# Optimization experiments

Hardware: AMD Instinct MI355X
Metric: run time of the kernel (lower is better)

The kernel has to match this reference:

```python
import jax, jax.numpy as jnp
import numpy as np

FEAT_STRIDE = 16
PRE_NMS = 6000   # TEST config
POST_NMS = 300
NMS_TH = 0.7


def _generate_anchors_3d(base_size=16, ratios=(0.5, 1.0, 2.0), scales=(8, 16, 32), time_dims=(16,)):
    """Standard Faster-RCNN anchor enumeration, extended with a time extent.
    Returns (A, 6) float32 boxes in [x1, y1, z1, x2, y2, z2] order (matches shift order)."""
    w = h = float(base_size)
    xc = yc = 0.5 * (base_size - 1)
    size = w * h
    ratios = np.asarray(ratios, dtype=np.float64)
    ws = np.round(np.sqrt(size / ratios))
    hs = np.round(ws * ratios)
    a2 = []
    for wi, hi in zip(ws, hs):
        for s in scales:
            ww, hh = wi * s, hi * s
            a2.append([xc - 0.5 * (ww - 1), yc - 0.5 * (hh - 1),
                       xc + 0.5 * (ww - 1), yc + 0.5 * (hh - 1)])
    out = []
    for t in time_dims:
        for a in a2:
            out.append([a[0], a[1], 0.0, a[2], a[3], float(t) - 1.0])
    return np.asarray(out, dtype=np.float32)


def setup_inputs() -> dict:
    key = jax.random.key(0)
    k1, k2 = jax.random.split(key)
    B, A, H, W, T = 2, 9, 32, 32, 16
    scores_map = jax.random.normal(k1, (B, 2 * A, H, W, T), dtype=jnp.float32)
    bbox_frame = jax.random.normal(k2, (B, 6 * A, H, W, T), dtype=jnp.float32) * 0.2
    im_info = jnp.array([512.0, 512.0, 16.0], dtype=jnp.float32)  # [img_h, img_w, n_frames]
    anchors = jnp.asarray(_generate_anchors_3d())  # (9, 6)
    return {"scores_map": scores_map, "bbox_frame": bbox_frame, "im_info": im_info, "anchors": anchors}


def _nms_single(boxes, scs):
    """Greedy 3D (spatio-temporal volume) NMS for one image.
    boxes: (N, 6), scs: (N,). Returns (POST_NMS, 7) rows [score, x1,y1,z1,x2,y2,z2],
    zero-padded past the number of kept proposals (matches output[i].zero_() + fill)."""
    order = jnp.argsort(-scs)[:PRE_NMS]           # descending score, pre-NMS top-k
    b = boxes[order]                              # (P, 6)
    s = scs[order]                                # (P,)
    vol = (b[:, 3] - b[:, 0] + 1.0) * (b[:, 4] - b[:, 1] + 1.0) * (b[:, 5] - b[:, 2] + 1.0)
    iw = jnp.clip(jnp.minimum(b[:, None, 3], b[None, :, 3]) - jnp.maximum(b[:, None, 0], b[None, :, 0]) + 1.0, 0.0)
    ih = jnp.clip(jnp.minimum(b[:, None, 4], b[None, :, 4]) - jnp.maximum(b[:, None, 1], b[None, :, 1]) + 1.0, 0.0)
    il = jnp.clip(jnp.minimum(b[:, None, 5], b[None, :, 5]) - jnp.maximum(b[:, None, 2], b[None, :, 2]) + 1.0, 0.0)
    inter = iw * ih * il                          # (P, P)
    iou = inter / (vol[:, None] + vol[None, :] - inter)
    iou = jax.lax.stop_gradient(iou)              # keep mask is non-differentiable
    P = b.shape[0]
    idx = jnp.arange(P)

    def step(keep, i):
        sup = (iou[i] > NMS_TH) & keep[i] & (idx > i)
        return keep & ~sup, None

    keep, _ = jax.lax.scan(step, jnp.ones((P,), dtype=bool), jnp.arange(P))
    rank = jnp.cumsum(keep) - 1
    pos = jnp.where(keep & (rank < POST_NMS), rank, POST_NMS)  # overflow slot POST_NMS
    rows = jnp.concatenate([s[:, None], b], axis=1)            # (P, 7)
    out = jnp.zeros((POST_NMS + 1, 7), dtype=boxes.dtype).at[pos].set(rows)
    return out[:POST_NMS]


def reference(scores_map, bbox_frame, im_info, anchors):
    A = anchors.shape[0]
    B = scores_map.shape[0]
    scores = scores_map[:, A:]                    # (B, A, H, W, T) foreground scores
    H, W, T = scores.shape[2], scores.shape[3], scores.shape[4]

    # --- anchor grid (matches np.meshgrid 'xy' + ravel = H-major, W, T order) ---
    sx = (jnp.arange(W) * FEAT_STRIDE).astype(scores_map.dtype)
    sy = (jnp.arange(H) * FEAT_STRIDE).astype(scores_map.dtype)
    sz = jnp.arange(T).astype(scores_map.dtype)
    X, Y, Z = jnp.meshgrid(sx, sy, sz)            # each (H, W, T)
    shift = jnp.stack([X.ravel(), Y.ravel(), Z.ravel()], axis=1)   # (K, 3)
    shifts = jnp.concatenate([shift, shift], axis=1)               # (K, 6)
    all_anchors = (anchors[None] + shifts[:, None]).reshape(-1, 6)  # (K*A, 6)

    deltas = bbox_frame.transpose(0, 2, 3, 4, 1).reshape(B, -1, 6)  # (B, K*A, 6)
    scs = scores.transpose(0, 2, 3, 4, 1).reshape(B, -1)            # (B, K*A)

    # --- bbox_transform_inv_3d ---
    aw = all_anchors[:, 3] - all_anchors[:, 0] + 1.0
    ah = all_anchors[:, 4] - all_anchors[:, 1] + 1.0
    al = all_anchors[:, 5] - all_anchors[:, 2] + 1.0
    acx = all_anchors[:, 0] + 0.5 * aw
    acy = all_anchors[:, 1] + 0.5 * ah
    acz = all_anchors[:, 2] + 0.5 * al
    pcx = deltas[..., 0] * aw + acx
    pcy = deltas[..., 1] * ah + acy
    pcz = deltas[..., 2] * al + acz
    pw = jnp.exp(deltas[..., 3]) * aw
    ph = jnp.exp(deltas[..., 4]) * ah
    pl = jnp.exp(deltas[..., 5]) * al
    proposals = jnp.stack([pcx - 0.5 * pw, pcy - 0.5 * ph, pcz - 0.5 * pl,
                           pcx + 0.5 * pw, pcy + 0.5 * ph, pcz + 0.5 * pl], axis=-1)

    # --- clip_boxes_3d: x in [0, img_w-1], y in [0, img_h-1], z in [0, n_frames-1] ---
    lim = jnp.stack([im_info[1], im_info[0], im_info[2],
                     im_info[1], im_info[0], im_info[2]]) - 1.0
    proposals = jnp.clip(proposals, 0.0, lim)

    return jax.vmap(_nms_single)(proposals, scs)  # (B, POST_NMS, 7)
```

## Files before the change

kernel.cpp:

```cpp
#include <hip/hip_runtime.h>
#include <stdint.h>

#define FEAT_STRIDE 16
#define PRE_NMS 6000
#define POST_NMS 300
#define NMS_TH 0.7f

static constexpr int B_ = 2, A_ = 9, H_ = 32, W_ = 32, T_ = 16;
static constexpr int LOC = H_ * W_ * T_;
static constexpr int N_ = LOC * A_;
static constexpr int NBIN = 65536;
static constexpr int NREP = 8;
static constexpr int CAP = 8192;
static constexpr int NW = 94;
static constexpr int ROWS = 6016;

static constexpr double BMID = 0.7000000178813934326171875;


__device__ __forceinline__ uint32_t f2u(float f) {
    uint32_t b = __float_as_uint(f);
    return b ^ ((b >> 31) ? 0xFFFFFFFFu : 0x80000000u);
}
__device__ __forceinline__ float u2f(uint32_t u) {
    uint32_t b = (u >> 31) ? (u ^ 0x80000000u) : ~u;
    return __uint_as_float(b);
}

__global__ void hist_kernel(const float* __restrict__ scores_map,
                            unsigned int* __restrict__ histR) {
    int gid = blockIdx.x * blockDim.x + threadIdx.x;
    if (gid >= B_ * N_) return;
    int b = gid / N_;
    int r = gid - b * N_;
    int a = r / LOC;
    int loc = r - a * LOC;
    float sc = scores_map[((size_t)(b * 2 * A_ + A_ + a)) * LOC + loc];
    uint32_t u = f2u(sc);
    int rep = blockIdx.x & (NREP - 1);
    atomicAdd(&histR[((size_t)(rep * B_ + b)) * NBIN + (u >> 16)], 1u);
}

__global__ void __launch_bounds__(256) partial_kernel(
        const unsigned int* __restrict__ histR,
        unsigned int* __restrict__ partials) {
    int c = blockIdx.x, bb = blockIdx.y, t = threadIdx.x;
    unsigned int s = 0;
#pragma unroll
    for (int r = 0; r < NREP; ++r) {
        const uint4* h4 = reinterpret_cast<const uint4*>(
            histR + ((size_t)(r * B_ + bb)) * NBIN + c * 1024);
        uint4 v = h4[t];
        s += v.x + v.y + v.z + v.w;
    }
    __shared__ unsigned int red[256];
    red[t] = s;
    __syncthreads();
    for (int off = 128; off > 0; off >>= 1) {
        if (t < off) red[t] += red[t + off];
        __syncthreads();
    }
    if (t == 0) partials[bb * 64 + c] = red[0];
}

__global__ void __launch_bounds__(256) rewrite_kernel(
        const unsigned int* __restrict__ histR,
        unsigned int* __restrict__ hist,
        unsigned int* __restrict__ binbase,
        const unsigned int* __restrict__ partials,
        unsigned int* __restrict__ thr) {
    int c = blockIdx.x, bb = blockIdx.y, t = threadIdx.x;
    __shared__ unsigned int sp[64];
    __shared__ unsigned int ssum[256];
    if (t < 64) sp[t] = partials[bb * 64 + t];
    uint4 v = {0u, 0u, 0u, 0u};
#pragma unroll
    for (int r = 0; r < NREP; ++r) {
        const uint4* h4 = reinterpret_cast<const uint4*>(
            histR + ((size_t)(r * B_ + bb)) * NBIN + c * 1024);
        uint4 w = h4[t];
        v.x += w.x; v.y += w.y; v.z += w.z; v.w += w.w;
    }
    unsigned int* h = hist + (size_t)bb * NBIN + c * 1024;
    unsigned int* bs = binbase + (size_t)bb * NBIN + c * 1024;
    ssum[t] = v.x + v.y + v.z + v.w;
    __syncthreads();
    unsigned int chunkBase = 0;
    for (int q = c + 1; q < 64; ++q) chunkBase += sp[q];
    for (int off = 1; off < 256; off <<= 1) {
        unsigned int val = (t + off < 256) ? ssum[t + off] : 0u;
        __syncthreads();
        ssum[t] += val;
        __syncthreads();
    }
    unsigned int run = chunkBase + ((t < 255) ? ssum[t + 1] : 0u);
    unsigned int cnt[4] = {v.x, v.y, v.z, v.w};
    unsigned int offv[4];
    for (int q = 3; q >= 0; --q) {
        offv[q] = run;
        unsigned int newrun = run + cnt[q];
        if (run < (unsigned)PRE_NMS && newrun >= (unsigned)PRE_NMS) {
            thr[bb * 2 + 0] = (unsigned)(c * 1024 + t * 4 + q);
            thr[bb * 2 + 1] = newrun;
        }
        run = newrun;
    }
    uint4 o4 = {offv[0], offv[1], offv[2], offv[3]};
    reinterpret_cast<uint4*>(h)[t] = o4;
    reinterpret_cast<uint4*>(bs)[t] = o4;
}

__global__ void __launch_bounds__(256) compact_kernel(
        const float* __restrict__ scores_map,
        const unsigned int* __restrict__ thr,
        unsigned long long* __restrict__ cand,
        unsigned int* __restrict__ hist) {
    int tid = threadIdx.x;
    int gid = blockIdx.x * 256 + tid;
    int b = gid / N_;
    int r = gid - b * N_;
    int a = r / LOC;
    int loc = r - a * LOC;
    float sc = scores_map[((size_t)(b * 2 * A_ + A_ + a)) * LOC + loc];
    uint32_t u = f2u(sc);
    uint32_t bin = u >> 16;
    if (bin >= thr[b * 2]) {
        int n = loc * A_ + a;
        unsigned long long key = ((unsigned long long)u << 18)
                               | (unsigned long long)(N_ - 1 - n);
        unsigned int slot = atomicAdd(&hist[b * NBIN + bin], 1u);
        if (slot < (unsigned)CAP)
            cand[(size_t)b * CAP + slot] = key;
    }
}

__global__ void __launch_bounds__(256) bucket_decode(
        const unsigned long long* __restrict__ cand,
        const unsigned int* __restrict__ hist,
        const unsigned int* __restrict__ binbase,
        const unsigned int* __restrict__ thr,
        const float* __restrict__ bbox_frame,
        const float* __restrict__ im_info,
        const float* __restrict__ anchors,
        float* __restrict__ sortedBox) {
    int gid = blockIdx.x * 256 + threadIdx.x;
    int bb = gid / CAP;
    int i = gid - bb * CAP;
    int count = (int)thr[bb * 2 + 1];
    if (count > CAP) count = CAP;
    if (i >= count) return;
    const unsigned long long* cb = cand + (size_t)bb * CAP;
    unsigned long long me = cb[i];
    int bin = (int)(me >> 34);
    int start = (int)binbase[bb * NBIN + bin];
    int end = (int)hist[bb * NBIN + bin];
    if (end > count) end = count;
    int rank = start;
    for (int q = start; q < end; ++q)
        rank += (cb[q] > me);
    if (rank >= PRE_NMS) return;

    uint32_t u = (uint32_t)(me >> 18);
    int n = N_ - 1 - (int)(me & 0x3FFFFull);
    int a = n % A_;
    int loc = n / A_;
    int k = loc % T_;
    int j = (loc / T_) % W_;
    int ii = loc / (T_ * W_);

    float ax1 = anchors[a * 6 + 0] + (float)(FEAT_STRIDE * j);
    float ay1 = anchors[a * 6 + 1] + (float)(FEAT_STRIDE * ii);
    float az1 = anchors[a * 6 + 2] + (float)k;
    float ax2 = anchors[a * 6 + 3] + (float)(FEAT_STRIDE * j);
    float ay2 = anchors[a * 6 + 4] + (float)(FEAT_STRIDE * ii);
    float az2 = anchors[a * 6 + 5] + (float)k;
    float aw = ax2 - ax1 + 1.0f, ah = ay2 - ay1 + 1.0f, al = az2 - az1 + 1.0f;
    float acx = ax1 + 0.5f * aw, acy = ay1 + 0.5f * ah, acz = az1 + 0.5f * al;

    const float* dp = bbox_frame + ((size_t)(bb * 6 * A_ + a * 6)) * LOC
                    + ii * (W_ * T_) + j * T_ + k;
    float d0 = dp[0 * LOC], d1 = dp[1 * LOC], d2 = dp[2 * LOC];
    float d3 = dp[3 * LOC], d4 = dp[4 * LOC], d5 = dp[5 * LOC];

    float pcx = d0 * aw + acx, pcy = d1 * ah + acy, pcz = d2 * al + acz;
    float pw = expf(d3) * aw, ph = expf(d4) * ah, pl = expf(d5) * al;

    float x1 = pcx - 0.5f * pw, y1 = pcy - 0.5f * ph, z1 = pcz - 0.5f * pl;
    float x2 = pcx + 0.5f * pw, y2 = pcy + 0.5f * ph, z2 = pcz + 0.5f * pl;

    float lx = im_info[1] - 1.0f, ly = im_info[0] - 1.0f, lz = im_info[2] - 1.0f;
    x1 = fminf(fmaxf(x1, 0.0f), lx); y1 = fminf(fmaxf(y1, 0.0f), ly); z1 = fminf(fmaxf(z1, 0.0f), lz);
    x2 = fminf(fmaxf(x2, 0.0f), lx); y2 = fminf(fmaxf(y2, 0.0f), ly); z2 = fminf(fmaxf(z2, 0.0f), lz);

    float vol = (x2 - x1 + 1.0f) * (y2 - y1 + 1.0f) * (z2 - z1 + 1.0f);
    float* p = sortedBox + ((size_t)bb * ROWS + rank) * 8;
    p[0] = x1; p[1] = y1; p[2] = z1; p[3] = x2;
    p[4] = y2; p[5] = z2; p[6] = vol; p[7] = u2f(u);
}

__global__ void mask_build(const float* __restrict__ sortedBox,
                           unsigned long long* __restrict__ mask,
                           unsigned long long* __restrict__ diagBand) {
    int g = blockIdx.x / NW, w = blockIdx.x % NW;
    if (w < g) return;
    int bb = blockIdx.y;
    int lane = threadIdx.x;
    __shared__ float4 colA[64];
    __shared__ float4 colB[64];
    const float* sb = sortedBox + (size_t)bb * ROWS * 8;
    int col = w * 64 + lane;
    if (col < PRE_NMS) {
        const float4* cp4 = reinterpret_cast<const float4*>(sb + (size_t)col * 8);
        float4 lo = cp4[0], hi = cp4[1];
        colA[lane] = make_float4(lo.x, lo.y, lo.z, lo.w);
        colB[lane] = make_float4(hi.x, hi.y, hi.z, 0.0f);
    } else {
        colA[lane] = make_float4(3e8f, 0.0f, 0.0f, -3e8f);
        colB[lane] = make_float4(0.0f, 0.0f, 1.0f, 0.0f);
    }
    __syncthreads();
    int row = g * 64 + lane;
    if (row >= PRE_NMS) return;
    const float4* rp4 = reinterpret_cast<const float4*>(sb + (size_t)row * 8);
    float4 rlo = rp4[0], rhi = rp4[1];
    float x1 = rlo.x, y1 = rlo.y, z1 = rlo.z;
    float x2 = rlo.w, y2 = rhi.x, z2 = rhi.y, v = rhi.z;
    unsigned long long word = 0;
#pragma unroll 8
    for (int b2 = 0; b2 < 64; ++b2) {
        float4 cA = colA[b2];
        float4 cB = colB[b2];
        float iw = fminf(x2, cA.w) - fmaxf(x1, cA.x) + 1.0f;
        float ih = fminf(y2, cB.x) - fmaxf(y1, cA.y) + 1.0f;
        float il = fminf(z2, cB.y) - fmaxf(z1, cA.z) + 1.0f;
        iw = fmaxf(iw, 0.0f); ih = fmaxf(ih, 0.0f); il = fmaxf(il, 0.0f);
        float inter = iw * ih * il;
        float denom = v + cB.z - inter;
        bool over = ((double)inter >= BMID * (double)denom);
        int cidx = w * 64 + b2;
        if (cidx > row && over) word |= (1ull << b2);
    }
    mask[((size_t)bb * NW + w) * ROWS + row] = word;
    if (w == g) {
        diagBand[((size_t)bb * ROWS + row) * 2 + 0] = word;
        if (g == NW - 1) diagBand[((size_t)bb * ROWS + row) * 2 + 1] = 0ull;
    }
    if (w == g + 1) diagBand[((size_t)bb * ROWS + row) * 2 + 1] = word;
}

__global__ void __launch_bounds__(1024) suppress_kernel(
        const unsigned long long* __restrict__ mask,
        const unsigned long long* __restrict__ diagBand,
        const float* __restrict__ sortedBox,
        float* __restrict__ out) {
    int bb = blockIdx.x;
    int tid = threadIdx.x;
    int lane = tid & 63;
    __shared__ unsigned long long remv[NW];
    __shared__ int kr[2][64];
    __shared__ int s_nk;
    for (int i = tid; i < NW; i += 1024) remv[i] = 0ull;
    if (tid == 0) {
        remv[NW - 1] = ~((1ull << (PRE_NMS - (NW - 1) * 64)) - 1ull);
        s_nk = 0;
    }
    __syncthreads();

    const unsigned long long* M = mask + (size_t)bb * NW * ROWS;
    const unsigned long long* D = diagBand + (size_t)bb * ROWS * 2;
    const float* sb = sortedBox + (size_t)bb * ROWS * 8;
    float* ob = out + (size_t)bb * POST_NMS * 7;

    int kept_total = 0, prev_nk = 0, prev_base = 0, cur = 0;
    unsigned long long diag0 = 0, band1 = 0, sup = 0;
    if (tid < 64) {
        diag0 = D[lane * 2 + 0];
        band1 = D[lane * 2 + 1];
    }

    for (int c = 0; c < NW; ++c) {
        unsigned long long nxt0 = 0, nxt1 = 0;
        if (tid < 64) {
            if (c + 1 < NW) {
                nxt0 = D[((c + 1) * 64 + lane) * 2 + 0];
                nxt1 = D[((c + 1) * 64 + lane) * 2 + 1];
            }
            unsigned long long alive = ~(remv[c] | sup);
            unsigned long long supn = 0;
            int nk = 0;
            while (alive && kept_total + nk < POST_NMS) {
                int b = __builtin_ctzll(alive);
                if (lane == 0) kr[cur][nk] = c * 64 + b;
                ++nk;
                alive &= ~(__shfl(diag0, b) | (1ull << b));
                supn |= __shfl(band1, b);
            }
            sup = supn;
            if (tid == 0) s_nk = nk;
        } else {
            int t = tid - 64;
            for (int w2 = c + 1 + t; w2 < NW; w2 += 960) {
                unsigned long long vv = remv[w2];
                for (int i = 0; i < prev_nk; ++i)
                    vv |= M[(size_t)w2 * ROWS + kr[cur ^ 1][i]];
                remv[w2] = vv;
            }
            for (int e = t; e < prev_nk * 7; e += 960) {
                int i = e / 7, j = e - i * 7;
                ob[(size_t)(prev_base + i) * 7 + j] =
                    sb[(size_t)kr[cur ^ 1][i] * 8 + (j == 0 ? 7 : j - 1)];
            }
        }
        __syncthreads();
        int nk = s_nk;
        prev_base = kept_total;
        kept_total += nk;
        prev_nk = nk;
        cur ^= 1;
        if (tid < 64) { diag0 = nxt0; band1 = nxt1; }
        if (kept_total >= POST_NMS) break;
    }
    for (int e = tid; e < prev_nk * 7; e += 1024) {
        int i = e / 7, j = e - i * 7;
        ob[(size_t)(prev_base + i) * 7 + j] =
            sb[(size_t)kr[cur ^ 1][i] * 8 + (j == 0 ? 7 : j - 1)];
    }
    for (int idx = kept_total * 7 + tid; idx < POST_NMS * 7; idx += 1024)
        ob[idx] = 0.0f;
}

extern "C" void kernel_launch(void* const* d_in, const int* in_sizes, int n_in,
                              void* d_out, int out_size, void* d_ws, size_t ws_size,
                              hipStream_t stream) {
    const float* scores_map = (const float*)d_in[0];
    const float* bbox_frame = (const float*)d_in[1];
    const float* im_info    = (const float*)d_in[2];
    const float* anchors    = (const float*)d_in[3];
    float* out = (float*)d_out;

    char* ws = (char*)d_ws;
    unsigned long long* mask     = (unsigned long long*)(ws + 0);
    unsigned int* binbase        = (unsigned int*)(ws + 0);
    unsigned int* histR          = (unsigned int*)(ws + 524288);
    float* sortedBox             = (float*)(ws + 9048064);
    unsigned long long* cand     = (unsigned long long*)(ws + 9433088);
    unsigned int* hist           = (unsigned int*)(ws + 9564160);
    unsigned long long* diagBand = (unsigned long long*)(ws + 9564160);
    unsigned int* thr            = (unsigned int*)(ws + 10088448);
    unsigned int* partials       = (unsigned int*)(ws + 10088464);

    hipMemsetAsync(histR, 0, (size_t)NREP * B_ * NBIN * 4, stream);

    int total = B_ * N_;
    hist_kernel<<<(total + 255) / 256, 256, 0, stream>>>(scores_map, histR);
    partial_kernel<<<dim3(64, B_), 256, 0, stream>>>(histR, partials);
    rewrite_kernel<<<dim3(64, B_), 256, 0, stream>>>(histR, hist, binbase, partials, thr);
    compact_kernel<<<total / 256, 256, 0, stream>>>(scores_map, thr, cand, hist);
    bucket_decode<<<B_ * CAP / 256, 256, 0, stream>>>(cand, hist, binbase, thr,
                                                      bbox_frame, im_info, anchors,
                                                      sortedBox);
    mask_build<<<dim3(NW * NW, B_), 64, 0, stream>>>(sortedBox, mask, diagBand);
    suppress_kernel<<<B_, 1024, 0, stream>>>(mask, diagBand, sortedBox, out);
}
```

Measured before the change: 134.1 us.

## Pipeline NMS suppress loop with a two-word band and deferred mask merging

The diagonal band grows to three 64-bit words per row, so suppression from the next two chunks is handled inside the 64-lane wave. That frees the other threads to fetch mask words for a chunk one iteration early and OR them into shared remv one iteration later with LDS atomics. The serial greedy loop now uses readfirstlane/readlane instead of shuffles and a raw s_barrier. Output rows are written once at the end from a shared kept-index list. This removes global-load latency and output writes from the critical serial path, at the cost of a larger band buffer and more register state.

Measured after the change: 138.6 us. +3.3%, slower.

```diff
diff --git a/kernel.cpp b/kernel.cpp
--- a/kernel.cpp
+++ b/kernel.cpp
@@ -25,6 +25,11 @@
 __device__ __forceinline__ float u2f(uint32_t u) {
     uint32_t b = (u >> 31) ? (u ^ 0x80000000u) : ~u;
     return __uint_as_float(b);
+}
+__device__ __forceinline__ unsigned long long rl64(unsigned long long v, int lane) {
+    unsigned int lo = (unsigned int)__builtin_amdgcn_readlane((int)(unsigned int)v, lane);
+    unsigned int hi = (unsigned int)__builtin_amdgcn_readlane((int)(unsigned int)(v >> 32), lane);
+    return ((unsigned long long)hi << 32) | lo;
 }
 
 __global__ void hist_kernel(const float* __restrict__ scores_map,
@@ -200,7 +205,7 @@
 
 __global__ void mask_build(const float* __restrict__ sortedBox,
                            unsigned long long* __restrict__ mask,
-                           unsigned long long* __restrict__ diagBand) {
+                           unsigned long long* __restrict__ band) {
     int g = blockIdx.x / NW, w = blockIdx.x % NW;
     if (w < g) return;
     int bb = blockIdx.y;
@@ -241,91 +246,122 @@
         if (cidx > row && over) word |= (1ull << b2);
     }
     mask[((size_t)bb * NW + w) * ROWS + row] = word;
+    unsigned long long* bd = band + ((size_t)bb * ROWS + row) * 4;
     if (w == g) {
-        diagBand[((size_t)bb * ROWS + row) * 2 + 0] = word;
-        if (g == NW - 1) diagBand[((size_t)bb * ROWS + row) * 2 + 1] = 0ull;
-    }
-    if (w == g + 1) diagBand[((size_t)bb * ROWS + row) * 2 + 1] = word;
+        bd[0] = word;
+        if (g + 1 >= NW) bd[1] = 0ull;
+        if (g + 2 >= NW) bd[2] = 0ull;
+    }
+    if (w == g + 1) bd[1] = word;
+    if (w == g + 2) bd[2] = word;
 }
 
 __global__ void __launch_bounds__(1024) suppress_kernel(
         const unsigned long long* __restrict__ mask,
-        const unsigned long long* __restrict__ diagBand,
+        const unsigned long long* __restrict__ band,
         const float* __restrict__ sortedBox,
         float* __restrict__ out) {
     int bb = blockIdx.x;
     int tid = threadIdx.x;
     int lane = tid & 63;
     __shared__ unsigned long long remv[NW];
-    __shared__ int kr[2][64];
-    __shared__ int s_nk;
+    __shared__ int kr[3][64];
+    __shared__ int keptAll[POST_NMS];
+    __shared__ int snk[3];
+    __shared__ int stot[2];
     for (int i = tid; i < NW; i += 1024) remv[i] = 0ull;
     if (tid == 0) {
         remv[NW - 1] = ~((1ull << (PRE_NMS - (NW - 1) * 64)) - 1ull);
-        s_nk = 0;
+        snk[0] = snk[1] = snk[2] = 0;
     }
     __syncthreads();
 
-    const unsigned long long* M = mask + (size_t)bb * NW * ROWS;
-    const unsigned long long* D = diagBand + (size_t)bb * ROWS * 2;
+    const unsigned long long* M  = mask + (size_t)bb * NW * ROWS;
+    const unsigned long long* Bd = band + (size_t)bb * ROWS * 4;
     const float* sb = sortedBox + (size_t)bb * ROWS * 8;
     float* ob = out + (size_t)bb * POST_NMS * 7;
 
-    int kept_total = 0, prev_nk = 0, prev_base = 0, cur = 0;
-    unsigned long long diag0 = 0, band1 = 0, sup = 0;
+    unsigned long long d0 = 0, d1 = 0, d2 = 0;
+    unsigned long long supCur = 0, S1 = 0, S2 = 0;
+    unsigned long long pend[8];
+    int kept_total = 0;
     if (tid < 64) {
-        diag0 = D[lane * 2 + 0];
-        band1 = D[lane * 2 + 1];
-    }
-
+        const ulonglong2* bp = reinterpret_cast<const ulonglong2*>(&Bd[(size_t)lane * 4]);
+        ulonglong2 v01 = bp[0], v23 = bp[1];
+        d0 = v01.x; d1 = v01.y; d2 = v23.x;
+    }
+
+    int total = 0;
     for (int c = 0; c < NW; ++c) {
-        unsigned long long nxt0 = 0, nxt1 = 0;
         if (tid < 64) {
+            unsigned long long n0 = 0, n1 = 0, n2 = 0;
             if (c + 1 < NW) {
-                nxt0 = D[((c + 1) * 64 + lane) * 2 + 0];
-                nxt1 = D[((c + 1) * 64 + lane) * 2 + 1];
+                const ulonglong2* bp = reinterpret_cast<const ulonglong2*>(
+                    &Bd[(size_t)((c + 1) * 64 + lane) * 4]);
+                ulonglong2 v01 = bp[0], v23 = bp[1];
+                n0 = v01.x; n1 = v01.y; n2 = v23.x;
             }
-            unsigned long long alive = ~(remv[c] | sup);
-            unsigned long long supn = 0;
+            unsigned long long alive = ~(remv[c] | supCur);
             int nk = 0;
             while (alive && kept_total + nk < POST_NMS) {
-                int b = __builtin_ctzll(alive);
-                if (lane == 0) kr[cur][nk] = c * 64 + b;
+                int b = (int)__builtin_ctzll(alive);
+                int bs = __builtin_amdgcn_readfirstlane(b);
+                unsigned long long dr = rl64(d0, bs);
+                if (lane == 0) {
+                    kr[c % 3][nk] = c * 64 + bs;
+                    keptAll[kept_total + nk] = c * 64 + bs;
+                }
+                S1 |= rl64(d1, bs);
+                S2 |= rl64(d2, bs);
                 ++nk;
-                alive &= ~(__shfl(diag0, b) | (1ull << b));
-                supn |= __shfl(band1, b);
+                alive &= ~(dr | (1ull << bs));
             }
-            sup = supn;
-            if (tid == 0) s_nk = nk;
+            kept_total += nk;
+            if (lane == 0) { snk[c % 3] = nk; stot[c & 1] = kept_total; }
+            supCur = S1; S1 = S2; S2 = 0;
+            d0 = n0; d1 = n1; d2 = n2;
         } else {
             int t = tid - 64;
-            for (int w2 = c + 1 + t; w2 < NW; w2 += 960) {
-                unsigned long long vv = remv[w2];
-                for (int i = 0; i < prev_nk; ++i)
-                    vv |= M[(size_t)w2 * ROWS + kr[cur ^ 1][i]];
-                remv[w2] = vv;
+            int wi = t >> 3, s = t & 7;
+            if (c >= 2) {
+                int t2 = c - 2;
+                int w = t2 + 3 + wi;
+                int nk2 = snk[t2 % 3];
+                if (w < NW && s < nk2) {
+                    unsigned long long acc = 0;
+#pragma unroll
+                    for (int q = 0; q < 8; ++q) {
+                        int i = s + q * 8;
+                        if (i < nk2) acc |= pend[q];
+                    }
+                    atomicOr(&remv[w], acc);
+                }
             }
-            for (int e = t; e < prev_nk * 7; e += 960) {
-                int i = e / 7, j = e - i * 7;
-                ob[(size_t)(prev_base + i) * 7 + j] =
-                    sb[(size_t)kr[cur ^ 1][i] * 8 + (j == 0 ? 7 : j - 1)];
+            if (c >= 1) {
+                int t1 = c - 1;
+                int w = t1 + 3 + wi;
+                int nk1 = snk[t1 % 3];
+                if (w < NW) {
+#pragma unroll
+                    for (int q = 0; q < 8; ++q) {
+                        int i = s + q * 8;
+                        if (i < nk1) pend[q] = M[(size_t)w * ROWS + kr[t1 % 3][i]];
+                    }
+                }
             }
         }
-        __syncthreads();
-        int nk = s_nk;
-        prev_base = kept_total;
-        kept_total += nk;
-        prev_nk = nk;
-        cur ^= 1;
-        if (tid < 64) { diag0 = nxt0; band1 = nxt1; }
-        if (kept_total >= POST_NMS) break;
-    }
-    for (int e = tid; e < prev_nk * 7; e += 1024) {
+        asm volatile("s_waitcnt lgkmcnt(0)" ::: "memory");
+        __builtin_amdgcn_s_barrier();
+        asm volatile("" ::: "memory");
+        total = stot[c & 1];
+        if (total >= POST_NMS) break;
+    }
+
+    for (int e = tid; e < total * 7; e += 1024) {
         int i = e / 7, j = e - i * 7;
-        ob[(size_t)(prev_base + i) * 7 + j] =
-            sb[(size_t)kr[cur ^ 1][i] * 8 + (j == 0 ? 7 : j - 1)];
-    }
-    for (int idx = kept_total * 7 + tid; idx < POST_NMS * 7; idx += 1024)
+        ob[e] = sb[(size_t)keptAll[i] * 8 + (j == 0 ? 7 : j - 1)];
+    }
+    for (int idx = total * 7 + tid; idx < POST_NMS * 7; idx += 1024)
         ob[idx] = 0.0f;
 }
 
@@ -339,15 +375,15 @@
     float* out = (float*)d_out;
 
     char* ws = (char*)d_ws;
-    unsigned long long* mask     = (unsigned long long*)(ws + 0);
-    unsigned int* binbase        = (unsigned int*)(ws + 0);
-    unsigned int* histR          = (unsigned int*)(ws + 524288);
-    float* sortedBox             = (float*)(ws + 9048064);
-    unsigned long long* cand     = (unsigned long long*)(ws + 9433088);
-    unsigned int* hist           = (unsigned int*)(ws + 9564160);
-    unsigned long long* diagBand = (unsigned long long*)(ws + 9564160);
-    unsigned int* thr            = (unsigned int*)(ws + 10088448);
-    unsigned int* partials       = (unsigned int*)(ws + 10088464);
+    unsigned long long* mask  = (unsigned long long*)(ws + 0);
+    unsigned int* binbase     = (unsigned int*)(ws + 0);
+    unsigned int* histR       = (unsigned int*)(ws + 524288);
+    float* sortedBox          = (float*)(ws + 9048064);
+    unsigned long long* cand  = (unsigned long long*)(ws + 9433088);
+    unsigned int* hist        = (unsigned int*)(ws + 9564160);
+    unsigned long long* band  = (unsigned long long*)(ws + 9564160);
+    unsigned int* thr         = (unsigned int*)(ws + 10088448);
+    unsigned int* partials    = (unsigned int*)(ws + 10088464);
 
     hipMemsetAsync(histR, 0, (size_t)NREP * B_ * NBIN * 4, stream);
 
@@ -359,6 +395,6 @@
     bucket_decode<<<B_ * CAP / 256, 256, 0, stream>>>(cand, hist, binbase, thr,
                                                       bbox_frame, im_info, anchors,
                                                       sortedBox);
-    mask_build<<<dim3(NW * NW, B_), 64, 0, stream>>>(sortedBox, mask, diagBand);
-    suppress_kernel<<<B_, 1024, 0, stream>>>(mask, diagBand, sortedBox, out);
-}
+    mask_build<<<dim3(NW * NW, B_), 64, 0, stream>>>(sortedBox, mask, band);
+    suppress_kernel<<<B_, 1024, 0, stream>>>(mask, band, sortedBox, out);
+}
```

## Process two mask words per suppress iteration and fuse histogram replica merge

Applied to the files above, without the earlier changes.

The greedy NMS suppress loop now handles two 64-column words per block-wide iteration, which halves the number of __syncthreads barriers on the serial critical path. To make that work, mask_build writes a 4-word band per row, so suppression from the previous pair reaches both current words. The greedy wave uses readfirstlane/readlane instead of shuffles. Separately, partial_kernel now writes the merged histogram so rewrite_kernel no longer re-reads all 8 replicas. The cost is more register state, a larger band buffer, and a longer serial inner step per iteration.

Result: slower. 136.9 us (+2.1%).

```diff
diff --git a/kernel.cpp b/kernel.cpp
--- a/kernel.cpp
+++ b/kernel.cpp
@@ -25,6 +25,11 @@
 __device__ __forceinline__ float u2f(uint32_t u) {
     uint32_t b = (u >> 31) ? (u ^ 0x80000000u) : ~u;
     return __uint_as_float(b);
+}
+__device__ __forceinline__ unsigned long long rl64(unsigned long long v, int lane) {
+    unsigned int lo = (unsigned int)__builtin_amdgcn_readlane((int)(unsigned int)v, lane);
+    unsigned int hi = (unsigned int)__builtin_amdgcn_readlane((int)(unsigned int)(v >> 32), lane);
+    return ((unsigned long long)hi << 32) | lo;
 }
 
 __global__ void hist_kernel(const float* __restrict__ scores_map,
@@ -43,18 +48,20 @@
 
 __global__ void __launch_bounds__(256) partial_kernel(
         const unsigned int* __restrict__ histR,
+        unsigned int* __restrict__ hist,
         unsigned int* __restrict__ partials) {
     int c = blockIdx.x, bb = blockIdx.y, t = threadIdx.x;
-    unsigned int s = 0;
+    uint4 acc = {0u, 0u, 0u, 0u};
 #pragma unroll
     for (int r = 0; r < NREP; ++r) {
         const uint4* h4 = reinterpret_cast<const uint4*>(
             histR + ((size_t)(r * B_ + bb)) * NBIN + c * 1024);
         uint4 v = h4[t];
-        s += v.x + v.y + v.z + v.w;
-    }
+        acc.x += v.x; acc.y += v.y; acc.z += v.z; acc.w += v.w;
+    }
+    reinterpret_cast<uint4*>(hist + (size_t)bb * NBIN + c * 1024)[t] = acc;
     __shared__ unsigned int red[256];
-    red[t] = s;
+    red[t] = acc.x + acc.y + acc.z + acc.w;
     __syncthreads();
     for (int off = 128; off > 0; off >>= 1) {
         if (t < off) red[t] += red[t + off];
@@ -64,7 +71,6 @@
 }
 
 __global__ void __launch_bounds__(256) rewrite_kernel(
-        const unsigned int* __restrict__ histR,
         unsigned int* __restrict__ hist,
         unsigned int* __restrict__ binbase,
         const unsigned int* __restrict__ partials,
@@ -73,16 +79,9 @@
     __shared__ unsigned int sp[64];
     __shared__ unsigned int ssum[256];
     if (t < 64) sp[t] = partials[bb * 64 + t];
-    uint4 v = {0u, 0u, 0u, 0u};
-#pragma unroll
-    for (int r = 0; r < NREP; ++r) {
-        const uint4* h4 = reinterpret_cast<const uint4*>(
-            histR + ((size_t)(r * B_ + bb)) * NBIN + c * 1024);
-        uint4 w = h4[t];
-        v.x += w.x; v.y += w.y; v.z += w.z; v.w += w.w;
-    }
     unsigned int* h = hist + (size_t)bb * NBIN + c * 1024;
     unsigned int* bs = binbase + (size_t)bb * NBIN + c * 1024;
+    uint4 v = reinterpret_cast<const uint4*>(h)[t];
     ssum[t] = v.x + v.y + v.z + v.w;
     __syncthreads();
     unsigned int chunkBase = 0;
@@ -200,7 +199,7 @@
 
 __global__ void mask_build(const float* __restrict__ sortedBox,
                            unsigned long long* __restrict__ mask,
-                           unsigned long long* __restrict__ diagBand) {
+                           unsigned long long* __restrict__ band) {
     int g = blockIdx.x / NW, w = blockIdx.x % NW;
     if (w < g) return;
     int bb = blockIdx.y;
@@ -241,23 +240,28 @@
         if (cidx > row && over) word |= (1ull << b2);
     }
     mask[((size_t)bb * NW + w) * ROWS + row] = word;
+    unsigned long long* bd = band + ((size_t)bb * ROWS + row) * 4;
     if (w == g) {
-        diagBand[((size_t)bb * ROWS + row) * 2 + 0] = word;
-        if (g == NW - 1) diagBand[((size_t)bb * ROWS + row) * 2 + 1] = 0ull;
-    }
-    if (w == g + 1) diagBand[((size_t)bb * ROWS + row) * 2 + 1] = word;
+        bd[0] = word;
+        if (g + 1 >= NW) bd[1] = 0ull;
+        if (g + 2 >= NW) bd[2] = 0ull;
+        if (g + 3 >= NW) bd[3] = 0ull;
+    }
+    if (w == g + 1) bd[1] = word;
+    if (w == g + 2) bd[2] = word;
+    if (w == g + 3) bd[3] = word;
 }
 
 __global__ void __launch_bounds__(1024) suppress_kernel(
         const unsigned long long* __restrict__ mask,
-        const unsigned long long* __restrict__ diagBand,
+        const unsigned long long* __restrict__ band,
         const float* __restrict__ sortedBox,
         float* __restrict__ out) {
     int bb = blockIdx.x;
     int tid = threadIdx.x;
     int lane = tid & 63;
     __shared__ unsigned long long remv[NW];
-    __shared__ int kr[2][64];
+    __shared__ int kr[2][128];
     __shared__ int s_nk;
     for (int i = tid; i < NW; i += 1024) remv[i] = 0ull;
     if (tid == 0) {
@@ -266,44 +270,76 @@
     }
     __syncthreads();
 
-    const unsigned long long* M = mask + (size_t)bb * NW * ROWS;
-    const unsigned long long* D = diagBand + (size_t)bb * ROWS * 2;
+    const unsigned long long* M  = mask + (size_t)bb * NW * ROWS;
+    const unsigned long long* Bd = band + (size_t)bb * ROWS * 4;
     const float* sb = sortedBox + (size_t)bb * ROWS * 8;
     float* ob = out + (size_t)bb * POST_NMS * 7;
 
     int kept_total = 0, prev_nk = 0, prev_base = 0, cur = 0;
-    unsigned long long diag0 = 0, band1 = 0, sup = 0;
+    unsigned long long dA0 = 0, dA1 = 0, dA2 = 0, dA3 = 0;
+    unsigned long long dB0 = 0, dB1 = 0, dB2 = 0, dB3 = 0;
+    unsigned long long sup0 = 0, sup1 = 0;
     if (tid < 64) {
-        diag0 = D[lane * 2 + 0];
-        band1 = D[lane * 2 + 1];
-    }
-
-    for (int c = 0; c < NW; ++c) {
-        unsigned long long nxt0 = 0, nxt1 = 0;
+        const ulonglong2* bp = reinterpret_cast<const ulonglong2*>(&Bd[(size_t)lane * 4]);
+        ulonglong2 u0 = bp[0], u1 = bp[1];
+        dA0 = u0.x; dA1 = u0.y; dA2 = u1.x; dA3 = u1.y;
+        const ulonglong2* bq = reinterpret_cast<const ulonglong2*>(&Bd[(size_t)(64 + lane) * 4]);
+        ulonglong2 v0 = bq[0], v1 = bq[1];
+        dB0 = v0.x; dB1 = v0.y; dB2 = v1.x; dB3 = v1.y;
+    }
+
+    const int NP = NW / 2;
+    for (int p = 0; p < NP; ++p) {
+        int w0 = 2 * p, w1 = 2 * p + 1;
         if (tid < 64) {
-            if (c + 1 < NW) {
-                nxt0 = D[((c + 1) * 64 + lane) * 2 + 0];
-                nxt1 = D[((c + 1) * 64 + lane) * 2 + 1];
-            }
-            unsigned long long alive = ~(remv[c] | sup);
-            unsigned long long supn = 0;
+            unsigned long long nA0 = 0, nA1 = 0, nA2 = 0, nA3 = 0;
+            unsigned long long nB0 = 0, nB1 = 0, nB2 = 0, nB3 = 0;
+            if (p + 1 < NP) {
+                const ulonglong2* bp2 = reinterpret_cast<const ulonglong2*>(
+                    &Bd[(size_t)((w0 + 2) * 64 + lane) * 4]);
+                ulonglong2 u0 = bp2[0], u1 = bp2[1];
+                nA0 = u0.x; nA1 = u0.y; nA2 = u1.x; nA3 = u1.y;
+                const ulonglong2* bq2 = reinterpret_cast<const ulonglong2*>(
+                    &Bd[(size_t)((w0 + 3) * 64 + lane) * 4]);
+                ulonglong2 v0 = bq2[0], v1 = bq2[1];
+                nB0 = v0.x; nB1 = v0.y; nB2 = v1.x; nB3 = v1.y;
+            }
+            unsigned long long S10 = 0, S11 = 0, w1sup = 0;
             int nk = 0;
+            unsigned long long alive = ~(remv[w0] | sup0);
             while (alive && kept_total + nk < POST_NMS) {
-                int b = __builtin_ctzll(alive);
-                if (lane == 0) kr[cur][nk] = c * 64 + b;
+                int b_ = (int)__builtin_ctzll(alive);
+                int bs = __builtin_amdgcn_readfirstlane(b_);
+                if (lane == 0) kr[cur][nk] = w0 * 64 + bs;
                 ++nk;
-                alive &= ~(__shfl(diag0, b) | (1ull << b));
-                supn |= __shfl(band1, b);
-            }
-            sup = supn;
-            if (tid == 0) s_nk = nk;
+                unsigned long long dr = rl64(dA0, bs);
+                w1sup |= rl64(dA1, bs);
+                S10   |= rl64(dA2, bs);
+                S11   |= rl64(dA3, bs);
+                alive &= ~(dr | (1ull << bs));
+            }
+            alive = ~(remv[w1] | sup1 | w1sup);
+            while (alive && kept_total + nk < POST_NMS) {
+                int b_ = (int)__builtin_ctzll(alive);
+                int bs = __builtin_amdgcn_readfirstlane(b_);
+                if (lane == 0) kr[cur][nk] = w1 * 64 + bs;
+                ++nk;
+                unsigned long long dr = rl64(dB0, bs);
+                S10 |= rl64(dB1, bs);
+                S11 |= rl64(dB2, bs);
+                alive &= ~(dr | (1ull << bs));
+            }
+            if (lane == 0) s_nk = nk;
+            sup0 = S10; sup1 = S11;
+            dA0 = nA0; dA1 = nA1; dA2 = nA2; dA3 = nA3;
+            dB0 = nB0; dB1 = nB1; dB2 = nB2; dB3 = nB3;
         } else {
             int t = tid - 64;
-            for (int w2 = c + 1 + t; w2 < NW; w2 += 960) {
-                unsigned long long vv = remv[w2];
+            for (int w2 = w0 + 2 + t; w2 < NW; w2 += 960) {
+                unsigned long long v = remv[w2];
                 for (int i = 0; i < prev_nk; ++i)
-                    vv |= M[(size_t)w2 * ROWS + kr[cur ^ 1][i]];
-                remv[w2] = vv;
+                    v |= M[(size_t)w2 * ROWS + kr[cur ^ 1][i]];
+                remv[w2] = v;
             }
             for (int e = t; e < prev_nk * 7; e += 960) {
                 int i = e / 7, j = e - i * 7;
@@ -317,7 +353,6 @@
         kept_total += nk;
         prev_nk = nk;
         cur ^= 1;
-        if (tid < 64) { diag0 = nxt0; band1 = nxt1; }
         if (kept_total >= POST_NMS) break;
     }
     for (int e = tid; e < prev_nk * 7; e += 1024) {
@@ -339,26 +374,26 @@
     float* out = (float*)d_out;
 
     char* ws = (char*)d_ws;
-    unsigned long long* mask     = (unsigned long long*)(ws + 0);
-    unsigned int* binbase        = (unsigned int*)(ws + 0);
-    unsigned int* histR          = (unsigned int*)(ws + 524288);
-    float* sortedBox             = (float*)(ws + 9048064);
-    unsigned long long* cand     = (unsigned long long*)(ws + 9433088);
-    unsigned int* hist           = (unsigned int*)(ws + 9564160);
-    unsigned long long* diagBand = (unsigned long long*)(ws + 9564160);
-    unsigned int* thr            = (unsigned int*)(ws + 10088448);
-    unsigned int* partials       = (unsigned int*)(ws + 10088464);
+    unsigned long long* mask  = (unsigned long long*)(ws + 0);
+    unsigned int* binbase     = (unsigned int*)(ws + 0);
+    unsigned int* histR       = (unsigned int*)(ws + 524288);
+    float* sortedBox          = (float*)(ws + 9048064);
+    unsigned long long* cand  = (unsigned long long*)(ws + 9433088);
+    unsigned int* hist        = (unsigned int*)(ws + 9564160);
+    unsigned long long* band  = (unsigned long long*)(ws + 9564160);
+    unsigned int* thr         = (unsigned int*)(ws + 10088448);
+    unsigned int* partials    = (unsigned int*)(ws + 10088464);
 
     hipMemsetAsync(histR, 0, (size_t)NREP * B_ * NBIN * 4, stream);
 
     int total = B_ * N_;
     hist_kernel<<<(total + 255) / 256, 256, 0, stream>>>(scores_map, histR);
-    partial_kernel<<<dim3(64, B_), 256, 0, stream>>>(histR, partials);
-    rewrite_kernel<<<dim3(64, B_), 256, 0, stream>>>(histR, hist, binbase, partials, thr);
+    partial_kernel<<<dim3(64, B_), 256, 0, stream>>>(histR, hist, partials);
+    rewrite_kernel<<<dim3(64, B_), 256, 0, stream>>>(hist, binbase, partials, thr);
     compact_kernel<<<total / 256, 256, 0, stream>>>(scores_map, thr, cand, hist);
     bucket_decode<<<B_ * CAP / 256, 256, 0, stream>>>(cand, hist, binbase, thr,
                                                       bbox_frame, im_info, anchors,
                                                       sortedBox);
-    mask_build<<<dim3(NW * NW, B_), 64, 0, stream>>>(sortedBox, mask, diagBand);
-    suppress_kernel<<<B_, 1024, 0, stream>>>(mask, diagBand, sortedBox, out);
-}
+    mask_build<<<dim3(NW * NW, B_), 64, 0, stream>>>(sortedBox, mask, band);
+    suppress_kernel<<<B_, 1024, 0, stream>>>(mask, band, sortedBox, out);
+}
```
